# Performance work log

Measured on AMD Instinct MI355X. Metric: run time of the kernel, lower is better.

## Reference

```python
import jax, jax.numpy as jnp
import numpy as np

B, M, N, K = 64, 1024, 1024, 128

def setup_inputs() -> dict:
    key = jax.random.key(0)
    k1, k2, k3 = jax.random.split(key, 3)
    # int8 operands (stored as int32 per spec; values fit in int8 range)
    a = jax.random.randint(k1, (B, M, K), 0, 127, dtype=jnp.int32)
    b = jax.random.randint(k2, (B, N, K), 0, 127, dtype=jnp.int32)  # S8N: N-major, matmul uses b^T
    alpha = jax.random.uniform(k3, (1,), dtype=jnp.float32) * 0.01
    return {"a": a, "b": b, "alpha": alpha}

def reference(a, b, alpha):
    acc = jnp.einsum('bmk,bnk->bmn', a, b)  # int32 accumulator
    # fused dequant epilogue: scale by alpha, cast to fp16
    return (alpha[0] * acc.astype(jnp.float32)).astype(jnp.float16)
```

## Files before the change

### kernel.cpp

```cpp
#include <hip/hip_runtime.h>


#define Mdim 1024
#define Ndim 1024
#define Kdim 128
#define TILE 128
#define LDS_STRIDE 144

using int32x4 = __attribute__((ext_vector_type(4))) int;
using floatx4 = __attribute__((ext_vector_type(4))) float;

__global__ __launch_bounds__(256)
void bmm_s8_kernel(const int* __restrict__ A, const int* __restrict__ Bm,
                   const float* __restrict__ alpha_p, float* __restrict__ out)
{
    __shared__ unsigned char As[TILE * LDS_STRIDE];
    __shared__ unsigned char Bs[TILE * LDS_STRIDE];

    const int t  = threadIdx.x;
    const int n0 = blockIdx.x * TILE;
    const int m0 = blockIdx.y * TILE;
    const int bz = blockIdx.z;

    const int* __restrict__ Ab = A  + (size_t)bz * Mdim * Kdim;
    const int* __restrict__ Bb = Bm + (size_t)bz * Ndim * Kdim;

#pragma unroll
    for (int j = 0; j < 16; ++j) {
        const int f    = t + 256 * j;
        const int row  = f >> 5;
        const int colb = (f & 31) * 4;

        const int32x4 va = *(const int32x4*)(Ab + (size_t)(m0 + row) * Kdim + colb);
        unsigned int pa = (unsigned)(va.x & 255)
                        | ((unsigned)(va.y & 255) << 8)
                        | ((unsigned)(va.z & 255) << 16)
                        | ((unsigned)(va.w & 255) << 24);
        *(unsigned int*)(&As[row * LDS_STRIDE + colb]) = pa;

        const int32x4 vb = *(const int32x4*)(Bb + (size_t)(n0 + row) * Kdim + colb);
        unsigned int pb = (unsigned)(vb.x & 255)
                        | ((unsigned)(vb.y & 255) << 8)
                        | ((unsigned)(vb.z & 255) << 16)
                        | ((unsigned)(vb.w & 255) << 24);
        *(unsigned int*)(&Bs[row * LDS_STRIDE + colb]) = pb;
    }
    __syncthreads();

    const int lane = t & 63;
    const int wave = t >> 6;
    const int wm = (wave >> 1) * 64;
    const int wn = (wave & 1) * 64;

    int32x4 acc[4][4];
#pragma unroll
    for (int mt = 0; mt < 4; ++mt)
#pragma unroll
        for (int nt = 0; nt < 4; ++nt)
            acc[mt][nt] = (int32x4){0, 0, 0, 0};

    const int lrow = lane & 15;
    const int koff = (lane >> 4) * 16;

#pragma unroll
    for (int ks = 0; ks < 2; ++ks) {
        int32x4 af[4], bf[4];
#pragma unroll
        for (int mt = 0; mt < 4; ++mt)
            af[mt] = *(const int32x4*)(&As[(wm + mt * 16 + lrow) * LDS_STRIDE + ks * 64 + koff]);
#pragma unroll
        for (int nt = 0; nt < 4; ++nt)
            bf[nt] = *(const int32x4*)(&Bs[(wn + nt * 16 + lrow) * LDS_STRIDE + ks * 64 + koff]);
#pragma unroll
        for (int mt = 0; mt < 4; ++mt)
#pragma unroll
            for (int nt = 0; nt < 4; ++nt)
                acc[mt][nt] = __builtin_amdgcn_mfma_i32_16x16x64_i8(
                    bf[nt], af[mt], acc[mt][nt], 0, 0, 0);
    }

    const float alpha = alpha_p[0];
    const int cm = lane & 15;
    const int cn = (lane >> 4) * 4;
    float* __restrict__ Ob = out + (size_t)bz * Mdim * Ndim;

#pragma unroll
    for (int mt = 0; mt < 4; ++mt) {
        const size_t rowbase = (size_t)(m0 + wm + mt * 16 + cm) * Ndim;
#pragma unroll
        for (int nt = 0; nt < 4; ++nt) {
            const int col = n0 + wn + nt * 16 + cn;
            floatx4 v;
            v.x = alpha * (float)acc[mt][nt][0];
            v.y = alpha * (float)acc[mt][nt][1];
            v.z = alpha * (float)acc[mt][nt][2];
            v.w = alpha * (float)acc[mt][nt][3];
            *(floatx4*)(Ob + rowbase + col) = v;
        }
    }
}

extern "C" void kernel_launch(void* const* d_in, const int* in_sizes, int n_in,
                              void* d_out, int out_size, void* d_ws, size_t ws_size,
                              hipStream_t stream) {
    const int*   a     = (const int*)d_in[0];
    const int*   b     = (const int*)d_in[1];
    const float* alpha = (const float*)d_in[2];
    float*       out   = (float*)d_out;

    const int batch = in_sizes[0] / (Mdim * Kdim);
    dim3 grid(Ndim / TILE, Mdim / TILE, batch);
    bmm_s8_kernel<<<grid, 256, 0, stream>>>(a, b, alpha, out);
}
```

Baseline: 401.7 us.

## Loop over N tiles per block with A reuse and double-buffered B prefetch

Each block now owns one (batch, M-tile) pair. It keeps the A tile resident in LDS and iterates over all eight N tiles. The next B tile is prefetched into registers and written into a double-buffered LDS slot, so global loads overlap MFMA compute and stores. This cuts redundant A loads and launch count, but the grid shrinks to 512 blocks, which lowers parallelism and raises register pressure.

```diff
diff --git a/kernel.cpp b/kernel.cpp
--- a/kernel.cpp
+++ b/kernel.cpp
@@ -10,92 +10,114 @@
 using int32x4 = __attribute__((ext_vector_type(4))) int;
 using floatx4 = __attribute__((ext_vector_type(4))) float;
 
+__device__ __forceinline__ unsigned pack8(int32x4 v) {
+    return (unsigned)(v.x & 255) | ((unsigned)(v.y & 255) << 8)
+         | ((unsigned)(v.z & 255) << 16) | ((unsigned)(v.w & 255) << 24);
+}
+
 __global__ __launch_bounds__(256)
 void bmm_s8_kernel(const int* __restrict__ A, const int* __restrict__ Bm,
                    const float* __restrict__ alpha_p, float* __restrict__ out)
 {
     __shared__ unsigned char As[TILE * LDS_STRIDE];
-    __shared__ unsigned char Bs[TILE * LDS_STRIDE];
+    __shared__ unsigned char Bs[2][TILE * LDS_STRIDE];
 
-    const int t  = threadIdx.x;
-    const int n0 = blockIdx.x * TILE;
-    const int m0 = blockIdx.y * TILE;
-    const int bz = blockIdx.z;
+    const int t      = threadIdx.x;
+    const int z      = blockIdx.x;
+    const int m_tile = blockIdx.y;
+    const int m0     = m_tile * TILE;
 
-    const int* __restrict__ Ab = A  + (size_t)bz * Mdim * Kdim;
-    const int* __restrict__ Bb = Bm + (size_t)bz * Ndim * Kdim;
+    const int* __restrict__ Ab = A  + (size_t)z * Mdim * Kdim + (size_t)m0 * Kdim;
+    const int* __restrict__ Bb = Bm + (size_t)z * Ndim * Kdim;
+
+    const int lane = t & 63;
+    const int wave = t >> 6;
 
 #pragma unroll
     for (int j = 0; j < 16; ++j) {
         const int f    = t + 256 * j;
         const int row  = f >> 5;
         const int colb = (f & 31) * 4;
+        const int32x4 va = *(const int32x4*)(Ab + (size_t)row * Kdim + colb);
+        *(unsigned*)(&As[row * LDS_STRIDE + colb]) = pack8(va);
+    }
 
-        const int32x4 va = *(const int32x4*)(Ab + (size_t)(m0 + row) * Kdim + colb);
-        unsigned int pa = (unsigned)(va.x & 255)
-                        | ((unsigned)(va.y & 255) << 8)
-                        | ((unsigned)(va.z & 255) << 16)
-                        | ((unsigned)(va.w & 255) << 24);
-        *(unsigned int*)(&As[row * LDS_STRIDE + colb]) = pa;
+    int32x4 breg[16];
+#pragma unroll
+    for (int j = 0; j < 16; ++j) {
+        const int f    = t + 256 * j;
+        const int row  = f >> 5;
+        const int colb = (f & 31) * 4;
+        breg[j] = *(const int32x4*)(Bb + (size_t)row * Kdim + colb);
+    }
 
-        const int32x4 vb = *(const int32x4*)(Bb + (size_t)(n0 + row) * Kdim + colb);
-        unsigned int pb = (unsigned)(vb.x & 255)
-                        | ((unsigned)(vb.y & 255) << 8)
-                        | ((unsigned)(vb.z & 255) << 16)
-                        | ((unsigned)(vb.w & 255) << 24);
-        *(unsigned int*)(&Bs[row * LDS_STRIDE + colb]) = pb;
-    }
-    __syncthreads();
-
-    const int lane = t & 63;
-    const int wave = t >> 6;
-    const int wm = (wave >> 1) * 64;
-    const int wn = (wave & 1) * 64;
-
-    int32x4 acc[4][4];
-#pragma unroll
-    for (int mt = 0; mt < 4; ++mt)
-#pragma unroll
-        for (int nt = 0; nt < 4; ++nt)
-            acc[mt][nt] = (int32x4){0, 0, 0, 0};
-
+    const float alpha = alpha_p[0];
+    const int wm   = (wave >> 1) * 64;
+    const int wn   = (wave & 1) * 64;
     const int lrow = lane & 15;
     const int koff = (lane >> 4) * 16;
+    const int cm   = lane & 15;
+    const int cn   = (lane >> 4) * 4;
+    float* __restrict__ Ob = out + (size_t)z * Mdim * Ndim;
 
+    for (int ni = 0; ni < 8; ++ni) {
+        const int buf = ni & 1;
 #pragma unroll
-    for (int ks = 0; ks < 2; ++ks) {
-        int32x4 af[4], bf[4];
+        for (int j = 0; j < 16; ++j) {
+            const int f    = t + 256 * j;
+            const int row  = f >> 5;
+            const int colb = (f & 31) * 4;
+            *(unsigned*)(&Bs[buf][row * LDS_STRIDE + colb]) = pack8(breg[j]);
+        }
+        if (ni < 7) {
+            const int* __restrict__ Bt = Bb + (size_t)(ni + 1) * TILE * Kdim;
 #pragma unroll
-        for (int mt = 0; mt < 4; ++mt)
-            af[mt] = *(const int32x4*)(&As[(wm + mt * 16 + lrow) * LDS_STRIDE + ks * 64 + koff]);
-#pragma unroll
-        for (int nt = 0; nt < 4; ++nt)
-            bf[nt] = *(const int32x4*)(&Bs[(wn + nt * 16 + lrow) * LDS_STRIDE + ks * 64 + koff]);
+            for (int j = 0; j < 16; ++j) {
+                const int f    = t + 256 * j;
+                const int row  = f >> 5;
+                const int colb = (f & 31) * 4;
+                breg[j] = *(const int32x4*)(Bt + (size_t)row * Kdim + colb);
+            }
+        }
+        __syncthreads();
+
+        int32x4 acc[4][4];
 #pragma unroll
         for (int mt = 0; mt < 4; ++mt)
 #pragma unroll
             for (int nt = 0; nt < 4; ++nt)
-                acc[mt][nt] = __builtin_amdgcn_mfma_i32_16x16x64_i8(
-                    bf[nt], af[mt], acc[mt][nt], 0, 0, 0);
-    }
-
-    const float alpha = alpha_p[0];
-    const int cm = lane & 15;
-    const int cn = (lane >> 4) * 4;
-    float* __restrict__ Ob = out + (size_t)bz * Mdim * Ndim;
+                acc[mt][nt] = (int32x4){0, 0, 0, 0};
 
 #pragma unroll
-    for (int mt = 0; mt < 4; ++mt) {
-        const size_t rowbase = (size_t)(m0 + wm + mt * 16 + cm) * Ndim;
+        for (int ks = 0; ks < 2; ++ks) {
+            int32x4 af[4], bf[4];
 #pragma unroll
-        for (int nt = 0; nt < 4; ++nt) {
-            const int col = n0 + wn + nt * 16 + cn;
-            floatx4 v;
-            v.x = alpha * (float)acc[mt][nt][0];
-            v.y = alpha * (float)acc[mt][nt][1];
-            v.z = alpha * (float)acc[mt][nt][2];
-            v.w = alpha * (float)acc[mt][nt][3];
-            *(floatx4*)(Ob + rowbase + col) = v;
+            for (int mt = 0; mt < 4; ++mt)
+                af[mt] = *(const int32x4*)(&As[(wm + mt * 16 + lrow) * LDS_STRIDE + ks * 64 + koff]);
+#pragma unroll
+            for (int nt = 0; nt < 4; ++nt)
+                bf[nt] = *(const int32x4*)(&Bs[buf][(wn + nt * 16 + lrow) * LDS_STRIDE + ks * 64 + koff]);
+#pragma unroll
+            for (int mt = 0; mt < 4; ++mt)
+#pragma unroll
+                for (int nt = 0; nt < 4; ++nt)
+                    acc[mt][nt] = __builtin_amdgcn_mfma_i32_16x16x64_i8(
+                        bf[nt], af[mt], acc[mt][nt], 0, 0, 0);
+        }
+
+#pragma unroll
+        for (int mt = 0; mt < 4; ++mt) {
+            const size_t rowbase = (size_t)(m0 + wm + mt * 16 + cm) * Ndim;
+#pragma unroll
+            for (int nt = 0; nt < 4; ++nt) {
+                const int col = ni * TILE + wn + nt * 16 + cn;
+                floatx4 v;
+                v.x = alpha * (float)acc[mt][nt][0];
+                v.y = alpha * (float)acc[mt][nt][1];
+                v.z = alpha * (float)acc[mt][nt][2];
+                v.w = alpha * (float)acc[mt][nt][3];
+                *(floatx4*)(Ob + rowbase + col) = v;
+            }
         }
     }
 }
@@ -109,6 +131,6 @@
     float*       out   = (float*)d_out;
 
     const int batch = in_sizes[0] / (Mdim * Kdim);
-    dim3 grid(Ndim / TILE, Mdim / TILE, batch);
+    dim3 grid(batch, Mdim / TILE);
     bmm_s8_kernel<<<grid, 256, 0, stream>>>(a, b, alpha, out);
 }
```

Measured after the change: 348.2 us. 13.3% less time.
